# Performance work log

Measured on AMD Instinct MI355X. Metric: run time of the kernel, lower is better.

The kernel has to match this reference:

```python
import jax, jax.numpy as jnp
import numpy as np

N, E, F, H = 100000, 1600000, 128, 128


def setup_inputs() -> dict:
    key = jax.random.key(0)
    ks = jax.random.split(key, 32)
    def w(i, shape):
        fan_in = shape[0]
        return jax.random.normal(ks[i], shape, dtype=jnp.float32) / np.sqrt(fan_in)
    inp = {
        'x': jax.random.normal(ks[0], (N, F), dtype=jnp.float32),
        't': jax.random.randint(ks[1], (N,), 0, 2, dtype=jnp.int32),
        'z': jax.random.normal(ks[2], (N, H), dtype=jnp.float32),
        'edge_index': jax.random.randint(ks[3], (2, E), 0, N, dtype=jnp.int32),
        # GCNConv weights (PyG: out = scatter(norm * (xW)) + b)
        'W_o': w(4, (F, H)), 'b_o': jnp.zeros((H,), jnp.float32),
        'W_t': w(5, (F, H)), 'b_t': jnp.zeros((H,), jnp.float32),
        # masked attention: Linear(2H, 1)
        'a_w': w(6, (2 * H, 1)), 'a_b': jnp.zeros((1,), jnp.float32),
        # encoder_final: Linear(2H, H)
        'W_enc': w(7, (2 * H, H)), 'b_enc': jnp.zeros((H,), jnp.float32),
        # predictor heads (3 linears each)
        'p1_W1': w(8, (H, H)), 'p1_b1': jnp.zeros((H,), jnp.float32),
        'p1_W2': w(9, (H, H)), 'p1_b2': jnp.zeros((H,), jnp.float32),
        'p1_W3': w(10, (H, 1)), 'p1_b3': jnp.zeros((1,), jnp.float32),
        'p0_W1': w(11, (H, H)), 'p0_b1': jnp.zeros((H,), jnp.float32),
        'p0_W2': w(12, (H, H)), 'p0_b2': jnp.zeros((H,), jnp.float32),
        'p0_W3': w(13, (H, 1)), 'p0_b3': jnp.zeros((1,), jnp.float32),
        # discriminator head
        'd_W1': w(14, (H, H)), 'd_b1': jnp.zeros((H,), jnp.float32),
        'd_W2': w(15, (H, H)), 'd_b2': jnp.zeros((H,), jnp.float32),
        'd_W3': w(16, (H, 1)), 'd_b3': jnp.zeros((1,), jnp.float32),
    }
    return inp


def _mlp3(x, W1, b1, W2, b2, W3, b3):
    h = jax.nn.leaky_relu(x @ W1 + b1, 0.2)
    h = jax.nn.leaky_relu(h @ W2 + b2, 0.2)
    return h @ W3 + b3


def _gcn(x, W, b, src, dst, norm, n):
    xw = x @ W                                   # [N,H]
    agg = jax.ops.segment_sum(xw[src] * norm[:, None], dst, num_segments=n)
    return agg + b


def reference(x, t, z, edge_index, W_o, b_o, W_t, b_t, a_w, a_b, W_enc, b_enc,
              p1_W1, p1_b1, p1_W2, p1_b2, p1_W3, p1_b3,
              p0_W1, p0_b1, p0_W2, p0_b2, p0_W3, p0_b3,
              d_W1, d_b1, d_W2, d_b2, d_W3, d_b3):
    n = x.shape[0]
    src, dst = edge_index[0], edge_index[1]
    # --- GCN with self-loops and symmetric normalization ---
    loop = jnp.arange(n, dtype=src.dtype)
    src2 = jnp.concatenate([src, loop])
    dst2 = jnp.concatenate([dst, loop])
    deg = jax.ops.segment_sum(jnp.ones_like(dst2, jnp.float32), dst2, num_segments=n)
    dinv = jax.lax.rsqrt(deg)                    # deg >= 1 (self loops)
    norm = dinv[src2] * dinv[dst2]               # [E+N]
    r_o = jax.nn.relu(_gcn(x, W_o, b_o, src2, dst2, norm, n))
    r_t = jax.nn.relu(_gcn(x, W_t, b_t, src2, dst2, norm, n))
    cat = jnp.concatenate([r_o, r_t], axis=-1)   # [N,2H]
    # --- masked attention over edges: only treated sources attend ---
    e = (cat @ a_w + a_b)[:, 0]                  # [N]
    logits = jax.nn.leaky_relu(e[src] + e[dst], 0.2)   # [E]
    mask = (t[src] > 0).astype(jnp.float32)
    m = jax.ops.segment_max(logits, dst, num_segments=n)
    m = jnp.where(jnp.isfinite(m), m, 0.0)
    w = jnp.exp(logits - m[dst]) * mask
    denom = jax.ops.segment_sum(w, dst, num_segments=n) + 1e-16
    alpha = w / denom[dst]                       # [E]
    h = jax.ops.segment_sum(r_t[src] * alpha[:, None], dst, num_segments=n)  # [N,H]
    # --- heads ---
    z_enc = jnp.concatenate([r_o, h], axis=-1) @ W_enc + b_enc   # [N,H]
    pred_1 = _mlp3(z_enc, p1_W1, p1_b1, p1_W2, p1_b2, p1_W3, p1_b3)[:, 0]
    pred_0 = _mlp3(z_enc, p0_W1, p0_b1, p0_W2, p0_b2, p0_W3, p0_b3)[:, 0]
    pred = jnp.where(t > 0, pred_1, pred_0)[:, None]             # [N,1]
    pred_t = jax.nn.sigmoid(_mlp3(r_t, d_W1, d_b1, d_W2, d_b2, d_W3, d_b3))  # [N,1]
    return pred_t, pred, z_enc
```

## Files before the change

### kernel.cpp

```cpp
#include <hip/hip_runtime.h>
#include <hip/hip_bf16.h>
#include <math.h>


using bf16x8 = __attribute__((ext_vector_type(8))) short;
using s16x8  = __attribute__((ext_vector_type(8))) short;
using f32x4  = __attribute__((ext_vector_type(4))) float;

static __device__ __forceinline__ float lrelu02(float x) { return x > 0.f ? x : 0.2f * x; }

static __device__ __forceinline__ unsigned short f2bf(float f) {
    unsigned u = __float_as_uint(f);
    unsigned r = u + 0x7FFF + ((u >> 16) & 1);
    return (unsigned short)(r >> 16);
}
static __device__ __forceinline__ float bf2f(unsigned short h) {
    return __uint_as_float(((unsigned)h) << 16);
}
static __device__ __forceinline__ float bflo(unsigned u) { return __uint_as_float(u << 16); }
static __device__ __forceinline__ float bfhi(unsigned u) { return __uint_as_float(u & 0xFFFF0000u); }


__global__ void k_zero_i32(int* __restrict__ p, int n) {
    int i = blockIdx.x * blockDim.x + threadIdx.x;
    int stride = gridDim.x * blockDim.x;
    for (; i < n; i += stride) p[i] = 0;
}

__global__ __launch_bounds__(256) void k_bhist(const int* __restrict__ src,
                                               const int* __restrict__ dst,
                                               const int* __restrict__ t,
                                               int* __restrict__ bhist,
                                               int* __restrict__ bhist_m,
                                               int e, int shift) {
    __shared__ int h[256], hm[256];
    h[threadIdx.x] = 0; hm[threadIdx.x] = 0;
    __syncthreads();
    int i = blockIdx.x * blockDim.x + threadIdx.x;
    int stride = gridDim.x * blockDim.x;
    for (; i < e; i += stride) {
        int b = dst[i] >> shift;
        atomicAdd(&h[b], 1);
        if (t[src[i]] > 0) atomicAdd(&hm[b], 1);
    }
    __syncthreads();
    if (h[threadIdx.x]) atomicAdd(&bhist[threadIdx.x], h[threadIdx.x]);
    if (hm[threadIdx.x]) atomicAdd(&bhist_m[threadIdx.x], hm[threadIdx.x]);
}

__global__ __launch_bounds__(256) void k_scan2(const int* __restrict__ bhist,
                                               const int* __restrict__ bhist_m,
                                               int* __restrict__ bbase,
                                               int* __restrict__ bbase_m,
                                               int* __restrict__ bcur, int nb) {
    __shared__ int s[256];
    int t = threadIdx.x;
    int v = (t < nb) ? bhist[t] : 0;
    s[t] = v;
    __syncthreads();
    for (int off = 1; off < 256; off <<= 1) {
        int u = (t >= off) ? s[t - off] : 0;
        __syncthreads();
        s[t] += u;
        __syncthreads();
    }
    if (t < nb) { bbase[t] = s[t] - v; bcur[t] = s[t] - v; }
    if (t == nb - 1) bbase[nb] = s[t];
    __syncthreads();
    int v2 = (t < nb) ? bhist_m[t] : 0;
    s[t] = v2;
    __syncthreads();
    for (int off = 1; off < 256; off <<= 1) {
        int u = (t >= off) ? s[t - off] : 0;
        __syncthreads();
        s[t] += u;
        __syncthreads();
    }
    if (t < nb) bbase_m[t] = s[t] - v2;
    if (t == nb - 1) bbase_m[nb] = s[t];
}

__global__ __launch_bounds__(256) void k_fillB(const int* __restrict__ src,
                                               const int* __restrict__ dst,
                                               const int* __restrict__ t,
                                               int* __restrict__ bcur,
                                               int* __restrict__ ebuf,
                                               int e, int shift) {
    __shared__ int h[256];
    const int EPT = 16;
    int blk_base = blockIdx.x * 256 * EPT;
    h[threadIdx.x] = 0;
    __syncthreads();
    int pk[EPT], bk[EPT];
#pragma unroll
    for (int j = 0; j < EPT; ++j) {
        int i = blk_base + threadIdx.x + j * 256;
        if (i < e) {
            int s = src[i], d = dst[i];
            int b = d >> shift;
            bk[j] = b;
            int tb = (t[s] > 0) ? 1 : 0;
            pk[j] = s | ((d - (b << shift)) << 20) | (tb << 29);
            atomicAdd(&h[b], 1);
        } else bk[j] = -1;
    }
    __syncthreads();
    int cnt = h[threadIdx.x];
    int base = 0;
    if (cnt > 0) base = atomicAdd(&bcur[threadIdx.x], cnt);
    __syncthreads();
    h[threadIdx.x] = base;
    __syncthreads();
#pragma unroll
    for (int j = 0; j < EPT; ++j) {
        if (bk[j] >= 0) {
            int pos = atomicAdd(&h[bk[j]], 1);
            ebuf[pos] = pk[j];
        }
    }
}

__global__ __launch_bounds__(256) void k_sortC(const int* __restrict__ ebuf,
                                               const int* __restrict__ bbase,
                                               const int* __restrict__ bbase_m,
                                               int* __restrict__ indptr,
                                               int* __restrict__ indptr_m,
                                               float* __restrict__ dinv,
                                               int* __restrict__ out_all,
                                               int* __restrict__ out_m,
                                               int n, int shift, int NB) {
    __shared__ int cnt[512], cnt_m[512];
    __shared__ int cur[512], cur_m[512];
    __shared__ int tmp[256];
    int tid = threadIdx.x;
    int b = blockIdx.x;
    int lo = bbase[b], hi = bbase[b + 1];
    int lom = bbase_m[b];
    int dbase = b << shift;
    for (int j = tid; j < 512; j += 256) { cnt[j] = 0; cnt_m[j] = 0; }
    __syncthreads();
    for (int i = lo + tid; i < hi; i += 256) {
        int pk = ebuf[i];
        int dlo = (pk >> 20) & 511;
        atomicAdd(&cnt[dlo], 1);
        if (pk >> 29) atomicAdd(&cnt_m[dlo], 1);
    }
    __syncthreads();
    int c0 = cnt[2 * tid], c1 = cnt[2 * tid + 1];
    int ps = c0 + c1;
    tmp[tid] = ps;
    __syncthreads();
    for (int off = 1; off < 256; off <<= 1) {
        int u = (tid >= off) ? tmp[tid - off] : 0;
        __syncthreads();
        tmp[tid] += u;
        __syncthreads();
    }
    int pre = tmp[tid] - ps;
    cur[2 * tid] = pre;
    cur[2 * tid + 1] = pre + c0;
    __syncthreads();
    int m0 = cnt_m[2 * tid], m1 = cnt_m[2 * tid + 1];
    int psm = m0 + m1;
    tmp[tid] = psm;
    __syncthreads();
    for (int off = 1; off < 256; off <<= 1) {
        int u = (tid >= off) ? tmp[tid - off] : 0;
        __syncthreads();
        tmp[tid] += u;
        __syncthreads();
    }
    int prem = tmp[tid] - psm;
    cur_m[2 * tid] = prem;
    cur_m[2 * tid + 1] = prem + m0;
    __syncthreads();
    int nd = n - dbase; if (nd > 512) nd = 512;
    for (int j = tid; j < nd; j += 256) {
        indptr[dbase + j] = lo + cur[j];
        indptr_m[dbase + j] = lom + cur_m[j];
        dinv[dbase + j] = rsqrtf((float)cnt[j] + 1.0f);
    }
    if (b == 0 && tid == 0) {
        indptr[n] = bbase[NB];
        indptr_m[n] = bbase_m[NB];
    }
    __syncthreads();
    for (int i = lo + tid; i < hi; i += 256) {
        int pk = ebuf[i];
        int s = pk & 0xFFFFF;
        int dlo = (pk >> 20) & 511;
        int pos = lo + atomicAdd(&cur[dlo], 1);
        out_all[pos] = s;
        if (pk >> 29) {
            int pm = lom + atomicAdd(&cur_m[dlo], 1);
            out_m[pm] = s;
        }
    }
}


__global__ void k_cvt_pre(const float* __restrict__ x, const float* __restrict__ dinv,
                          unsigned short* __restrict__ xp, int total4) {
    int i = blockIdx.x * blockDim.x + threadIdx.x;
    int stride = gridDim.x * blockDim.x;
    for (; i < total4; i += stride) {
        float dv = dinv[i >> 5];
        float4 v = ((const float4*)x)[i];
        ushort4 o;
        o.x = f2bf(v.x * dv); o.y = f2bf(v.y * dv);
        o.z = f2bf(v.z * dv); o.w = f2bf(v.w * dv);
        ((ushort4*)xp)[i] = o;
    }
}

__global__ void k_wprep(const float* __restrict__ Wo, const float* __restrict__ Wti,
                        const float* __restrict__ Wenc,
                        const float* __restrict__ p1W1, const float* __restrict__ p1W2,
                        const float* __restrict__ p0W1, const float* __restrict__ p0W2,
                        const float* __restrict__ dW1, const float* __restrict__ dW2,
                        unsigned short* __restrict__ Wcat_t,
                        unsigned short* __restrict__ Wenc_t,
                        unsigned short* __restrict__ o1, unsigned short* __restrict__ o2,
                        unsigned short* __restrict__ o3, unsigned short* __restrict__ o4,
                        unsigned short* __restrict__ o5, unsigned short* __restrict__ o6) {
    int idx = blockIdx.x * 256 + threadIdx.x;
    if (idx < 32768) {
        int j = idx >> 7, k = idx & 127;
        float v = (j < 128) ? Wo[(k << 7) + j] : Wti[(k << 7) + j - 128];
        Wcat_t[idx] = f2bf(v);
    } else if (idx < 65536) {
        int i = idx - 32768;
        Wenc_t[(size_t)(i & 127) * 256 + (i >> 7)] = f2bf(Wenc[i]);
    } else {
        int i2 = idx - 65536;
        int h = i2 >> 14;
        int i = i2 & 16383;
        const float* W; unsigned short* O;
        switch (h) {
            case 0: W = p1W1; O = o1; break;
            case 1: W = p1W2; O = o2; break;
            case 2: W = p0W1; O = o3; break;
            case 3: W = p0W2; O = o4; break;
            case 4: W = dW1;  O = o5; break;
            default: W = dW2; O = o6; break;
        }
        O[(i & 127) * 128 + (i >> 7)] = f2bf(W[i]);
    }
}

__global__ __launch_bounds__(256) void k_aggx(const unsigned short* __restrict__ xp,
                                              const int* __restrict__ indptr,
                                              const int* __restrict__ srcs,
                                              const float* __restrict__ dinv,
                                              unsigned short* __restrict__ aggx, int n) {
    int wv = threadIdx.x >> 6, lane = threadIdx.x & 63;
    int v = blockIdx.x * 4 + wv;
    if (v >= n) return;
    const unsigned* xp2 = (const unsigned*)xp;
    int beg = indptr[v], end = indptr[v + 1];
    unsigned sv = xp2[(size_t)v * 64 + lane];
    float a0 = bflo(sv), a1 = bfhi(sv);
    int i = beg;
    for (; i + 8 <= end; i += 8) {
        int s0 = srcs[i], s1 = srcs[i + 1], s2 = srcs[i + 2], s3 = srcs[i + 3];
        int s4 = srcs[i + 4], s5 = srcs[i + 5], s6 = srcs[i + 6], s7 = srcs[i + 7];
        unsigned u0 = xp2[(size_t)s0 * 64 + lane];
        unsigned u1 = xp2[(size_t)s1 * 64 + lane];
        unsigned u2 = xp2[(size_t)s2 * 64 + lane];
        unsigned u3 = xp2[(size_t)s3 * 64 + lane];
        unsigned u4 = xp2[(size_t)s4 * 64 + lane];
        unsigned u5 = xp2[(size_t)s5 * 64 + lane];
        unsigned u6 = xp2[(size_t)s6 * 64 + lane];
        unsigned u7 = xp2[(size_t)s7 * 64 + lane];
        a0 += bflo(u0) + bflo(u1) + bflo(u2) + bflo(u3)
            + bflo(u4) + bflo(u5) + bflo(u6) + bflo(u7);
        a1 += bfhi(u0) + bfhi(u1) + bfhi(u2) + bfhi(u3)
            + bfhi(u4) + bfhi(u5) + bfhi(u6) + bfhi(u7);
    }
    for (; i + 4 <= end; i += 4) {
        int s0 = srcs[i], s1 = srcs[i + 1], s2 = srcs[i + 2], s3 = srcs[i + 3];
        unsigned u0 = xp2[(size_t)s0 * 64 + lane];
        unsigned u1 = xp2[(size_t)s1 * 64 + lane];
        unsigned u2 = xp2[(size_t)s2 * 64 + lane];
        unsigned u3 = xp2[(size_t)s3 * 64 + lane];
        a0 += bflo(u0) + bflo(u1) + bflo(u2) + bflo(u3);
        a1 += bfhi(u0) + bfhi(u1) + bfhi(u2) + bfhi(u3);
    }
    for (; i < end; ++i) {
        unsigned u = xp2[(size_t)srcs[i] * 64 + lane];
        a0 += bflo(u); a1 += bfhi(u);
    }
    float dv = dinv[v];
    a0 *= dv; a1 *= dv;
    unsigned o = (unsigned)f2bf(a0) | ((unsigned)f2bf(a1) << 16);
    ((unsigned*)aggx)[(size_t)v * 64 + lane] = o;
}

__global__ __launch_bounds__(256) void k_gcn(const unsigned short* __restrict__ aggx,
                                             const unsigned short* __restrict__ Wcat,
                                             const float* __restrict__ b_o,
                                             const float* __restrict__ b_t,
                                             const float* __restrict__ a_w,
                                             const float* __restrict__ a_b,
                                             unsigned short* __restrict__ cat2,
                                             unsigned short* __restrict__ rt,
                                             float* __restrict__ e, int M) {
    __shared__ short ct[64][264];
    int wave = threadIdx.x >> 6, lane = threadIdx.x & 63;
    int row_base = blockIdx.x * 64 + wave * 16;
    int rA = row_base + (lane & 15);
    if (rA >= M) rA = M - 1;
    int koff = (lane >> 4) << 3;
    int colL = lane & 15;

    bf16x8 a[4];
#pragma unroll
    for (int ks = 0; ks < 4; ++ks)
        a[ks] = *(const bf16x8*)((const short*)aggx + (size_t)rA * 128 + (ks << 5) + koff);

    f32x4 acc[16];
#pragma unroll
    for (int cf = 0; cf < 16; ++cf) acc[cf] = (f32x4){0.f, 0.f, 0.f, 0.f};
#pragma unroll
    for (int ks = 0; ks < 4; ++ks)
#pragma unroll
        for (int cf = 0; cf < 16; ++cf) {
            bf16x8 b = *(const bf16x8*)((const short*)Wcat + (size_t)((cf << 4) + colL) * 128 + (ks << 5) + koff);
            acc[cf] = __builtin_amdgcn_mfma_f32_16x16x32_bf16(a[ks], b, acc[cf], 0, 0, 0);
        }

    float ep0 = 0.f, ep1 = 0.f, ep2 = 0.f, ep3 = 0.f;
    int rl0 = wave * 16 + ((lane >> 4) << 2);
#pragma unroll
    for (int cf = 0; cf < 16; ++cf) {
        int col = (cf << 4) + colL;
        float bv = (col < 128) ? b_o[col] : b_t[col - 128];
        float aw = a_w[col];
#pragma unroll
        for (int j = 0; j < 4; ++j) {
            float v = fmaxf(acc[cf][j] + bv, 0.f);
            if (j == 0) ep0 += v * aw;
            else if (j == 1) ep1 += v * aw;
            else if (j == 2) ep2 += v * aw;
            else ep3 += v * aw;
            ct[rl0 + j][col] = (short)f2bf(v);
        }
    }
#pragma unroll
    for (int mk = 1; mk < 16; mk <<= 1) {
        ep0 += __shfl_xor(ep0, mk); ep1 += __shfl_xor(ep1, mk);
        ep2 += __shfl_xor(ep2, mk); ep3 += __shfl_xor(ep3, mk);
    }
    if (colL == 0) {
        float ab = a_b[0];
        int r0 = row_base + ((lane >> 4) << 2);
        if (r0 + 0 < M) e[r0 + 0] = ep0 + ab;
        if (r0 + 1 < M) e[r0 + 1] = ep1 + ab;
        if (r0 + 2 < M) e[r0 + 2] = ep2 + ab;
        if (r0 + 3 < M) e[r0 + 3] = ep3 + ab;
    }
    __syncthreads();
    int base64 = blockIdx.x * 64;
    short* cp = (short*)cat2 + (size_t)base64 * 256;
    for (int j = threadIdx.x; j < 1024; j += 256) {
        int row = j >> 4;
        if (base64 + row < M)
            *(s16x8*)(cp + (size_t)row * 256 + ((j & 15) << 3)) =
                *(const s16x8*)&ct[row][(j & 15) << 3];
    }
    short* rp = (short*)rt + (size_t)base64 * 128;
    for (int j = threadIdx.x; j < 1024; j += 256) {
        int row = j >> 4;
        if (base64 + row < M)
            *(s16x8*)(rp + (size_t)row * 128 + ((j & 15) << 3)) =
                *(const s16x8*)&ct[row][128 + ((j & 15) << 3)];
    }
}

__global__ __launch_bounds__(256) void k_attn(const unsigned short* __restrict__ rt,
                                              const int* __restrict__ indptr_m,
                                              const int* __restrict__ srcs_m,
                                              const float* __restrict__ e,
                                              unsigned short* __restrict__ cat2, int n) {
    int wv = threadIdx.x >> 6, lane = threadIdx.x & 63;
    int v = blockIdx.x * 4 + wv;
    if (v >= n) return;
    float ev = e[v];
    int bm = indptr_m[v], em = indptr_m[v + 1];
    float m = -INFINITY;
    for (int i = bm + lane; i < em; i += 64)
        m = fmaxf(m, lrelu02(ev + e[srcs_m[i]]));
    for (int off = 32; off; off >>= 1) m = fmaxf(m, __shfl_xor(m, off));
    if (bm == em) m = 0.f;
    float h0 = 0.f, h1 = 0.f, wsum = 0.f;
    const unsigned* rt2 = (const unsigned*)rt;
    int i = bm;
    for (; i + 8 <= em; i += 8) {
        int s0 = srcs_m[i], s1 = srcs_m[i + 1], s2 = srcs_m[i + 2], s3 = srcs_m[i + 3];
        int s4 = srcs_m[i + 4], s5 = srcs_m[i + 5], s6 = srcs_m[i + 6], s7 = srcs_m[i + 7];
        float w0 = __expf(lrelu02(ev + e[s0]) - m);
        float w1 = __expf(lrelu02(ev + e[s1]) - m);
        float w2 = __expf(lrelu02(ev + e[s2]) - m);
        float w3 = __expf(lrelu02(ev + e[s3]) - m);
        float w4 = __expf(lrelu02(ev + e[s4]) - m);
        float w5 = __expf(lrelu02(ev + e[s5]) - m);
        float w6 = __expf(lrelu02(ev + e[s6]) - m);
        float w7 = __expf(lrelu02(ev + e[s7]) - m);
        unsigned u0 = rt2[(size_t)s0 * 64 + lane];
        unsigned u1 = rt2[(size_t)s1 * 64 + lane];
        unsigned u2 = rt2[(size_t)s2 * 64 + lane];
        unsigned u3 = rt2[(size_t)s3 * 64 + lane];
        unsigned u4 = rt2[(size_t)s4 * 64 + lane];
        unsigned u5 = rt2[(size_t)s5 * 64 + lane];
        unsigned u6 = rt2[(size_t)s6 * 64 + lane];
        unsigned u7 = rt2[(size_t)s7 * 64 + lane];
        wsum += w0 + w1 + w2 + w3 + w4 + w5 + w6 + w7;
        h0 += w0 * bflo(u0) + w1 * bflo(u1) + w2 * bflo(u2) + w3 * bflo(u3)
            + w4 * bflo(u4) + w5 * bflo(u5) + w6 * bflo(u6) + w7 * bflo(u7);
        h1 += w0 * bfhi(u0) + w1 * bfhi(u1) + w2 * bfhi(u2) + w3 * bfhi(u3)
            + w4 * bfhi(u4) + w5 * bfhi(u5) + w6 * bfhi(u6) + w7 * bfhi(u7);
    }
    for (; i < em; ++i) {
        int s = srcs_m[i];
        float w = __expf(lrelu02(ev + e[s]) - m);
        unsigned u = rt2[(size_t)s * 64 + lane];
        wsum += w;
        h0 += w * bflo(u);
        h1 += w * bfhi(u);
    }
    float inv = 1.f / (wsum + 1e-16f);
    unsigned o = (unsigned)f2bf(h0 * inv) | ((unsigned)f2bf(h1 * inv) << 16);
    ((unsigned*)(cat2 + (size_t)v * 256 + 128))[lane] = o;
}

__global__ __launch_bounds__(512) void k_tail(
    const unsigned short* __restrict__ cat2, const unsigned short* __restrict__ rt_bf,
    const unsigned short* __restrict__ Wenc, const float* __restrict__ b_enc,
    const unsigned short* __restrict__ W11, const float* __restrict__ b11,
    const unsigned short* __restrict__ W12, const float* __restrict__ b12,
    const float* __restrict__ W13, const float* __restrict__ b13,
    const unsigned short* __restrict__ W01, const float* __restrict__ b01,
    const unsigned short* __restrict__ W02, const float* __restrict__ b02,
    const float* __restrict__ W03, const float* __restrict__ b03,
    const unsigned short* __restrict__ Wd1, const float* __restrict__ bd1,
    const unsigned short* __restrict__ Wd2, const float* __restrict__ bd2,
    const float* __restrict__ Wd3, const float* __restrict__ bd3,
    const int* __restrict__ t, float* __restrict__ zenc,
    float* __restrict__ out, int M) {
    __shared__ __align__(16) char pool[128 * 136 * 2 + 128 * 136 * 2];
    short* Wa = (short*)pool;
    short* hb = (short*)(pool + 128 * 136 * 2);
    float* zt = (float*)pool;

    int wave = threadIdx.x >> 6, lane = threadIdx.x & 63;
    int colL = lane & 15;
    int koff = (lane >> 4) << 3;
    int base128 = blockIdx.x * 128;
    int rA = base128 + wave * 16 + colL;
    if (rA >= M) rA = M - 1;

    bf16x8 ra[4];
#pragma unroll
    for (int ks = 0; ks < 4; ++ks)
        ra[ks] = *(const bf16x8*)((const short*)rt_bf + (size_t)rA * 128 + (ks << 5) + koff);

    f32x4 acc1[8];
    {
        const short* Ap = (const short*)cat2 + (size_t)rA * 256 + koff;
        const short* Bp = (const short*)Wenc + (size_t)colL * 256 + koff;
#pragma unroll
        for (int cf = 0; cf < 8; ++cf) acc1[cf] = (f32x4){0.f, 0.f, 0.f, 0.f};
#pragma unroll
        for (int ks = 0; ks < 8; ++ks) {
            bf16x8 a = *(const bf16x8*)(Ap + (ks << 5));
#pragma unroll
            for (int cf = 0; cf < 8; ++cf) {
                bf16x8 b = *(const bf16x8*)(Bp + (size_t)(cf << 4) * 256 + (ks << 5));
                acc1[cf] = __builtin_amdgcn_mfma_f32_16x16x32_bf16(a, b, acc1[cf], 0, 0, 0);
            }
        }
    }

    bf16x8 za[4];
#pragma unroll
    for (int chunk = 0; chunk < 2; ++chunk) {
        if ((wave >> 2) == chunk) {
            int rl0 = (wave & 3) * 16 + ((lane >> 4) << 2);
#pragma unroll
            for (int cf = 0; cf < 8; ++cf) {
                int col = (cf << 4) + colL;
                float bv = b_enc[col];
#pragma unroll
                for (int j = 0; j < 4; ++j)
                    zt[(rl0 + j) * 132 + col] = acc1[cf][j] + bv;
            }
        }
        __syncthreads();
        {
            int gbase = base128 + chunk * 64;
            float* zp = zenc + (size_t)gbase * 128;
            for (int j = threadIdx.x; j < 2048; j += 512) {
                int row = j >> 5;
                if (gbase + row < M)
                    *(float4*)(zp + (size_t)j * 4) = *(const float4*)&zt[row * 132 + ((j & 31) << 2)];
            }
        }
        if ((wave >> 2) == chunk) {
            int rAl = (wave & 3) * 16 + colL;
#pragma unroll
            for (int ks = 0; ks < 4; ++ks) {
                float4 v0 = *(const float4*)&zt[rAl * 132 + (ks << 5) + koff];
                float4 v1 = *(const float4*)&zt[rAl * 132 + (ks << 5) + koff + 4];
                za[ks][0] = (short)f2bf(v0.x); za[ks][1] = (short)f2bf(v0.y);
                za[ks][2] = (short)f2bf(v0.z); za[ks][3] = (short)f2bf(v0.w);
                za[ks][4] = (short)f2bf(v1.x); za[ks][5] = (short)f2bf(v1.y);
                za[ks][6] = (short)f2bf(v1.z); za[ks][7] = (short)f2bf(v1.w);
            }
        }
        __syncthreads();
    }

    float sp1[4], sp0[4], sdd[4];

    auto stage = [&](const unsigned short* W) {
        for (int i = threadIdx.x; i < 2048; i += 512) {
            int r = i >> 4, c = (i & 15) << 3;
            bf16x8 v = *(const bf16x8*)((const short*)W + (r << 7) + c);
            *(bf16x8*)(Wa + r * 136 + c) = v;
        }
    };

    auto run_head = [&](const bf16x8* A0,
                        const unsigned short* W1, const float* b1,
                        const unsigned short* W2, const float* b2,
                        const float* W3, const float* b3, float* sout) {
        __syncthreads();
        stage(W1);
        __syncthreads();
        f32x4 acc[8];
#pragma unroll
        for (int cf = 0; cf < 8; ++cf) acc[cf] = (f32x4){0.f, 0.f, 0.f, 0.f};
#pragma unroll
        for (int ks = 0; ks < 4; ++ks)
#pragma unroll
            for (int cf = 0; cf < 8; ++cf) {
                bf16x8 b = *(const bf16x8*)(Wa + ((cf << 4) + colL) * 136 + (ks << 5) + koff);
                acc[cf] = __builtin_amdgcn_mfma_f32_16x16x32_bf16(A0[ks], b, acc[cf], 0, 0, 0);
            }
        short* hw = hb + wave * 2176;
#pragma unroll
        for (int cf = 0; cf < 8; ++cf) {
            int col = (cf << 4) + colL;
            float bv = b1[col];
#pragma unroll
            for (int j = 0; j < 4; ++j)
                hw[(((lane >> 4) << 2) + j) * 136 + col] = (short)f2bf(lrelu02(acc[cf][j] + bv));
        }
        __syncthreads();
        stage(W2);
        __syncthreads();
        bf16x8 h1f[4];
#pragma unroll
        for (int ks = 0; ks < 4; ++ks)
            h1f[ks] = *(const bf16x8*)(hw + colL * 136 + (ks << 5) + koff);
#pragma unroll
        for (int cf = 0; cf < 8; ++cf) acc[cf] = (f32x4){0.f, 0.f, 0.f, 0.f};
#pragma unroll
        for (int ks = 0; ks < 4; ++ks)
#pragma unroll
            for (int cf = 0; cf < 8; ++cf) {
                bf16x8 b = *(const bf16x8*)(Wa + ((cf << 4) + colL) * 136 + (ks << 5) + koff);
                acc[cf] = __builtin_amdgcn_mfma_f32_16x16x32_bf16(h1f[ks], b, acc[cf], 0, 0, 0);
            }
        float s0 = 0.f, s1 = 0.f, s2 = 0.f, s3 = 0.f;
#pragma unroll
        for (int cf = 0; cf < 8; ++cf) {
            int col = (cf << 4) + colL;
            float w3 = W3[col], bv = b2[col];
            s0 += lrelu02(acc[cf][0] + bv) * w3;
            s1 += lrelu02(acc[cf][1] + bv) * w3;
            s2 += lrelu02(acc[cf][2] + bv) * w3;
            s3 += lrelu02(acc[cf][3] + bv) * w3;
        }
#pragma unroll
        for (int mk = 1; mk < 16; mk <<= 1) {
            s0 += __shfl_xor(s0, mk); s1 += __shfl_xor(s1, mk);
            s2 += __shfl_xor(s2, mk); s3 += __shfl_xor(s3, mk);
        }
        float bb = b3[0];
        sout[0] = s0 + bb; sout[1] = s1 + bb; sout[2] = s2 + bb; sout[3] = s3 + bb;
    };

    run_head(za, W11, b11, W12, b12, W13, b13, sp1);
    run_head(za, W01, b01, W02, b02, W03, b03, sp0);
    run_head(ra, Wd1, bd1, Wd2, bd2, Wd3, bd3, sdd);

    if (colL == 0) {
#pragma unroll
        for (int j = 0; j < 4; ++j) {
            int row = base128 + wave * 16 + ((lane >> 4) << 2) + j;
            if (row < M) {
                out[row] = 1.f / (1.f + __expf(-sdd[j]));
                out[M + row] = (t[row] > 0) ? sp1[j] : sp0[j];
            }
        }
    }
}


extern "C" void kernel_launch(void* const* d_in, const int* in_sizes, int n_in,
                              void* d_out, int out_size, void* d_ws, size_t ws_size,
                              hipStream_t stream) {
    const float* x     = (const float*)d_in[0];
    const int*   t     = (const int*)d_in[1];
    const int*   ei    = (const int*)d_in[3];
    const float* W_o   = (const float*)d_in[4];
    const float* b_o   = (const float*)d_in[5];
    const float* W_t   = (const float*)d_in[6];
    const float* b_t   = (const float*)d_in[7];
    const float* a_w   = (const float*)d_in[8];
    const float* a_b   = (const float*)d_in[9];
    const float* W_enc = (const float*)d_in[10];
    const float* b_enc = (const float*)d_in[11];
    const float* p1_W1 = (const float*)d_in[12]; const float* p1_b1 = (const float*)d_in[13];
    const float* p1_W2 = (const float*)d_in[14]; const float* p1_b2 = (const float*)d_in[15];
    const float* p1_W3 = (const float*)d_in[16]; const float* p1_b3 = (const float*)d_in[17];
    const float* p0_W1 = (const float*)d_in[18]; const float* p0_b1 = (const float*)d_in[19];
    const float* p0_W2 = (const float*)d_in[20]; const float* p0_b2 = (const float*)d_in[21];
    const float* p0_W3 = (const float*)d_in[22]; const float* p0_b3 = (const float*)d_in[23];
    const float* d_W1  = (const float*)d_in[24]; const float* d_b1  = (const float*)d_in[25];
    const float* d_W2  = (const float*)d_in[26]; const float* d_b2  = (const float*)d_in[27];
    const float* d_W3  = (const float*)d_in[28]; const float* d_b3  = (const float*)d_in[29];

    const int n = in_sizes[1];
    const int E = in_sizes[3] / 2;
    const int* src = ei;
    const int* dst = ei + E;

    float* out  = (float*)d_out;
    float* zenc = out + 2 * (size_t)n;

    const int shift = 9;
    const int NB = (n + (1 << shift) - 1) >> shift;

    char* base = (char*)d_ws;
    size_t o = 0;
    auto alloc = [&](size_t bytes) { char* p = base + o; o += (bytes + 255) & ~(size_t)255; return p; };
    unsigned short* xp_bf   = (unsigned short*)alloc((size_t)n * 128 * 2);
    unsigned short* aggx_bf = (unsigned short*)alloc((size_t)n * 128 * 2);
    unsigned short* cat2_bf = (unsigned short*)alloc((size_t)n * 256 * 2);
    unsigned short* rt_bf   = (unsigned short*)alloc((size_t)n * 128 * 2);
    float* dinv = (float*)alloc((size_t)n * 4);
    float* evec = (float*)alloc((size_t)n * 4);
    unsigned short* Wcat_t = (unsigned short*)alloc(256 * 128 * 2);
    unsigned short* Wenc_t = (unsigned short*)alloc(128 * 256 * 2);
    unsigned short* Wp1a_t = (unsigned short*)alloc(128 * 128 * 2);
    unsigned short* Wp1b_t = (unsigned short*)alloc(128 * 128 * 2);
    unsigned short* Wp0a_t = (unsigned short*)alloc(128 * 128 * 2);
    unsigned short* Wp0b_t = (unsigned short*)alloc(128 * 128 * 2);
    unsigned short* Wda_t  = (unsigned short*)alloc(128 * 128 * 2);
    unsigned short* Wdb_t  = (unsigned short*)alloc(128 * 128 * 2);
    int* indptr     = (int*)alloc(((size_t)n + 1) * 4);
    int* indptr_m   = (int*)alloc(((size_t)n + 1) * 4);
    int* bhist      = (int*)alloc(514 * 4);
    int* bhist_m    = bhist + 257;
    int* bbase      = (int*)alloc(257 * 4);
    int* bbase_m    = (int*)alloc(257 * 4);
    int* bcur       = (int*)alloc(257 * 4);
    int* src_sorted = (int*)alloc((size_t)E * 4);
    int* src_mask   = (int*)alloc((size_t)E * 4);
    int* ebuf       = (int*)alloc((size_t)E * 4);

    const int mt  = (n + 63) / 64;
    const int mt2 = (n + 127) / 128;

    k_zero_i32<<<1, 256, 0, stream>>>(bhist, 514);
    k_bhist<<<1024, 256, 0, stream>>>(src, dst, t, bhist, bhist_m, E, shift);
    k_scan2<<<1, 256, 0, stream>>>(bhist, bhist_m, bbase, bbase_m, bcur, NB);
    k_fillB<<<(E + 4095) / 4096, 256, 0, stream>>>(src, dst, t, bcur, ebuf, E, shift);
    k_sortC<<<NB, 256, 0, stream>>>(ebuf, bbase, bbase_m, indptr, indptr_m, dinv,
                                    src_sorted, src_mask, n, shift, NB);

    k_wprep<<<640, 256, 0, stream>>>(W_o, W_t, W_enc, p1_W1, p1_W2, p0_W1, p0_W2,
                                     d_W1, d_W2, Wcat_t, Wenc_t,
                                     Wp1a_t, Wp1b_t, Wp0a_t, Wp0b_t, Wda_t, Wdb_t);
    k_cvt_pre<<<2048, 256, 0, stream>>>(x, dinv, xp_bf, n * 32);

    k_aggx<<<(n + 3) / 4, 256, 0, stream>>>(xp_bf, indptr, src_sorted, dinv, aggx_bf, n);

    k_gcn<<<mt, 256, 0, stream>>>(aggx_bf, Wcat_t, b_o, b_t, a_w, a_b,
                                  cat2_bf, rt_bf, evec, n);

    k_attn<<<(n + 3) / 4, 256, 0, stream>>>(rt_bf, indptr_m, src_mask, evec, cat2_bf, n);

    k_tail<<<mt2, 512, 0, stream>>>(cat2_bf, rt_bf, Wenc_t, b_enc,
                                    Wp1a_t, p1_b1, Wp1b_t, p1_b2, p1_W3, p1_b3,
                                    Wp0a_t, p0_b1, Wp0b_t, p0_b2, p0_W3, p0_b3,
                                    Wda_t, d_b1, Wdb_t, d_b2, d_W3, d_b3,
                                    t, zenc, out, n);
}
```

Baseline: 428.8 us.

## Fuse neighbor aggregation into GCN matmul kernel via shared-memory staging

Merges the sparse neighbor-sum kernel into the GCN MFMA kernel. Each 64-row block first aggregates its own rows into an LDS tile, then feeds the matrix multiply from LDS. This removes the aggx intermediate write and read through global memory plus one launch. In exchange, each wave now processes 16 nodes serially instead of one node per wave, which reduces parallelism and the ability to hide gather latency. The extra LDS tile may also lower occupancy.

```diff
diff --git a/kernel.cpp b/kernel.cpp
--- a/kernel.cpp
+++ b/kernel.cpp
@@ -248,75 +248,75 @@
     }
 }
 
-__global__ __launch_bounds__(256) void k_aggx(const unsigned short* __restrict__ xp,
-                                              const int* __restrict__ indptr,
-                                              const int* __restrict__ srcs,
-                                              const float* __restrict__ dinv,
-                                              unsigned short* __restrict__ aggx, int n) {
-    int wv = threadIdx.x >> 6, lane = threadIdx.x & 63;
-    int v = blockIdx.x * 4 + wv;
-    if (v >= n) return;
-    const unsigned* xp2 = (const unsigned*)xp;
-    int beg = indptr[v], end = indptr[v + 1];
-    unsigned sv = xp2[(size_t)v * 64 + lane];
-    float a0 = bflo(sv), a1 = bfhi(sv);
-    int i = beg;
-    for (; i + 8 <= end; i += 8) {
-        int s0 = srcs[i], s1 = srcs[i + 1], s2 = srcs[i + 2], s3 = srcs[i + 3];
-        int s4 = srcs[i + 4], s5 = srcs[i + 5], s6 = srcs[i + 6], s7 = srcs[i + 7];
-        unsigned u0 = xp2[(size_t)s0 * 64 + lane];
-        unsigned u1 = xp2[(size_t)s1 * 64 + lane];
-        unsigned u2 = xp2[(size_t)s2 * 64 + lane];
-        unsigned u3 = xp2[(size_t)s3 * 64 + lane];
-        unsigned u4 = xp2[(size_t)s4 * 64 + lane];
-        unsigned u5 = xp2[(size_t)s5 * 64 + lane];
-        unsigned u6 = xp2[(size_t)s6 * 64 + lane];
-        unsigned u7 = xp2[(size_t)s7 * 64 + lane];
-        a0 += bflo(u0) + bflo(u1) + bflo(u2) + bflo(u3)
-            + bflo(u4) + bflo(u5) + bflo(u6) + bflo(u7);
-        a1 += bfhi(u0) + bfhi(u1) + bfhi(u2) + bfhi(u3)
-            + bfhi(u4) + bfhi(u5) + bfhi(u6) + bfhi(u7);
-    }
-    for (; i + 4 <= end; i += 4) {
-        int s0 = srcs[i], s1 = srcs[i + 1], s2 = srcs[i + 2], s3 = srcs[i + 3];
-        unsigned u0 = xp2[(size_t)s0 * 64 + lane];
-        unsigned u1 = xp2[(size_t)s1 * 64 + lane];
-        unsigned u2 = xp2[(size_t)s2 * 64 + lane];
-        unsigned u3 = xp2[(size_t)s3 * 64 + lane];
-        a0 += bflo(u0) + bflo(u1) + bflo(u2) + bflo(u3);
-        a1 += bfhi(u0) + bfhi(u1) + bfhi(u2) + bfhi(u3);
-    }
-    for (; i < end; ++i) {
-        unsigned u = xp2[(size_t)srcs[i] * 64 + lane];
-        a0 += bflo(u); a1 += bfhi(u);
-    }
-    float dv = dinv[v];
-    a0 *= dv; a1 *= dv;
-    unsigned o = (unsigned)f2bf(a0) | ((unsigned)f2bf(a1) << 16);
-    ((unsigned*)aggx)[(size_t)v * 64 + lane] = o;
-}
-
-__global__ __launch_bounds__(256) void k_gcn(const unsigned short* __restrict__ aggx,
-                                             const unsigned short* __restrict__ Wcat,
-                                             const float* __restrict__ b_o,
-                                             const float* __restrict__ b_t,
-                                             const float* __restrict__ a_w,
-                                             const float* __restrict__ a_b,
-                                             unsigned short* __restrict__ cat2,
-                                             unsigned short* __restrict__ rt,
-                                             float* __restrict__ e, int M) {
+__global__ __launch_bounds__(256) void k_agg_gcn(const unsigned short* __restrict__ xp,
+                                                 const int* __restrict__ indptr,
+                                                 const int* __restrict__ srcs,
+                                                 const float* __restrict__ dinv,
+                                                 const unsigned short* __restrict__ Wcat,
+                                                 const float* __restrict__ b_o,
+                                                 const float* __restrict__ b_t,
+                                                 const float* __restrict__ a_w,
+                                                 const float* __restrict__ a_b,
+                                                 unsigned short* __restrict__ cat2,
+                                                 unsigned short* __restrict__ rt,
+                                                 float* __restrict__ e, int M) {
+    __shared__ short at[64][136];
     __shared__ short ct[64][264];
     int wave = threadIdx.x >> 6, lane = threadIdx.x & 63;
-    int row_base = blockIdx.x * 64 + wave * 16;
-    int rA = row_base + (lane & 15);
-    if (rA >= M) rA = M - 1;
+    int base64 = blockIdx.x * 64;
+    const unsigned* xp2 = (const unsigned*)xp;
+
+    for (int nd = 0; nd < 16; ++nd) {
+        int v = base64 + wave * 16 + nd;
+        int vc = (v < M) ? v : M - 1;
+        int beg = indptr[vc], end = indptr[vc + 1];
+        unsigned sv = xp2[(size_t)vc * 64 + lane];
+        float a0 = bflo(sv), a1 = bfhi(sv);
+        int i = beg;
+        for (; i + 8 <= end; i += 8) {
+            int s0 = srcs[i], s1 = srcs[i + 1], s2 = srcs[i + 2], s3 = srcs[i + 3];
+            int s4 = srcs[i + 4], s5 = srcs[i + 5], s6 = srcs[i + 6], s7 = srcs[i + 7];
+            unsigned u0 = xp2[(size_t)s0 * 64 + lane];
+            unsigned u1 = xp2[(size_t)s1 * 64 + lane];
+            unsigned u2 = xp2[(size_t)s2 * 64 + lane];
+            unsigned u3 = xp2[(size_t)s3 * 64 + lane];
+            unsigned u4 = xp2[(size_t)s4 * 64 + lane];
+            unsigned u5 = xp2[(size_t)s5 * 64 + lane];
+            unsigned u6 = xp2[(size_t)s6 * 64 + lane];
+            unsigned u7 = xp2[(size_t)s7 * 64 + lane];
+            a0 += bflo(u0) + bflo(u1) + bflo(u2) + bflo(u3)
+                + bflo(u4) + bflo(u5) + bflo(u6) + bflo(u7);
+            a1 += bfhi(u0) + bfhi(u1) + bfhi(u2) + bfhi(u3)
+                + bfhi(u4) + bfhi(u5) + bfhi(u6) + bfhi(u7);
+        }
+        for (; i + 4 <= end; i += 4) {
+            int s0 = srcs[i], s1 = srcs[i + 1], s2 = srcs[i + 2], s3 = srcs[i + 3];
+            unsigned u0 = xp2[(size_t)s0 * 64 + lane];
+            unsigned u1 = xp2[(size_t)s1 * 64 + lane];
+            unsigned u2 = xp2[(size_t)s2 * 64 + lane];
+            unsigned u3 = xp2[(size_t)s3 * 64 + lane];
+            a0 += bflo(u0) + bflo(u1) + bflo(u2) + bflo(u3);
+            a1 += bfhi(u0) + bfhi(u1) + bfhi(u2) + bfhi(u3);
+        }
+        for (; i < end; ++i) {
+            unsigned u = xp2[(size_t)srcs[i] * 64 + lane];
+            a0 += bflo(u); a1 += bfhi(u);
+        }
+        float dv = dinv[vc];
+        a0 *= dv; a1 *= dv;
+        unsigned o = (unsigned)f2bf(a0) | ((unsigned)f2bf(a1) << 16);
+        ((unsigned*)&at[wave * 16 + nd][0])[lane] = o;
+    }
+    __syncthreads();
+
     int koff = (lane >> 4) << 3;
     int colL = lane & 15;
+    int row_base = base64 + wave * 16;
 
     bf16x8 a[4];
 #pragma unroll
     for (int ks = 0; ks < 4; ++ks)
-        a[ks] = *(const bf16x8*)((const short*)aggx + (size_t)rA * 128 + (ks << 5) + koff);
+        a[ks] = *(const bf16x8*)&at[wave * 16 + (lane & 15)][(ks << 5) + koff];
 
     f32x4 acc[16];
 #pragma unroll
@@ -360,7 +360,6 @@
         if (r0 + 3 < M) e[r0 + 3] = ep3 + ab;
     }
     __syncthreads();
-    int base64 = blockIdx.x * 64;
     short* cp = (short*)cat2 + (size_t)base64 * 256;
     for (int j = threadIdx.x; j < 1024; j += 256) {
         int row = j >> 4;
@@ -647,7 +646,6 @@
     size_t o = 0;
     auto alloc = [&](size_t bytes) { char* p = base + o; o += (bytes + 255) & ~(size_t)255; return p; };
     unsigned short* xp_bf   = (unsigned short*)alloc((size_t)n * 128 * 2);
-    unsigned short* aggx_bf = (unsigned short*)alloc((size_t)n * 128 * 2);
     unsigned short* cat2_bf = (unsigned short*)alloc((size_t)n * 256 * 2);
     unsigned short* rt_bf   = (unsigned short*)alloc((size_t)n * 128 * 2);
     float* dinv = (float*)alloc((size_t)n * 4);
@@ -686,10 +684,8 @@
                                      Wp1a_t, Wp1b_t, Wp0a_t, Wp0b_t, Wda_t, Wdb_t);
     k_cvt_pre<<<2048, 256, 0, stream>>>(x, dinv, xp_bf, n * 32);
 
-    k_aggx<<<(n + 3) / 4, 256, 0, stream>>>(xp_bf, indptr, src_sorted, dinv, aggx_bf, n);
-
-    k_gcn<<<mt, 256, 0, stream>>>(aggx_bf, Wcat_t, b_o, b_t, a_w, a_b,
-                                  cat2_bf, rt_bf, evec, n);
+    k_agg_gcn<<<mt, 256, 0, stream>>>(xp_bf, indptr, src_sorted, dinv, Wcat_t,
+                                      b_o, b_t, a_w, a_b, cat2_bf, rt_bf, evec, n);
 
     k_attn<<<(n + 3) / 4, 256, 0, stream>>>(rt_bf, indptr_m, src_mask, evec, cat2_bf, n);
 
```

Result: slower. 522.8 us (+21.9%).
